# Kernel tuning notes

Hardware: AMD Instinct MI355X
Metric: run time of the kernel (lower is better)

The kernel has to match this reference:

```python
import jax, jax.numpy as jnp
import numpy as np

K = 5          # number of spline bins
B = 5.0        # tail bound
HIDDEN = 8
MIN_W = 1e-3; MIN_H = 1e-3; MIN_D = 1e-3  # RQS defaults (Durkan et al.)


def setup_inputs() -> dict:
    n, d = 32768, 64
    L = d - 1
    P = 3 * K - 1
    ks = jax.random.split(jax.random.key(0), 8)
    x = jax.random.normal(ks[0], (n, d), jnp.float32) * 2.0
    init_param = jax.random.uniform(ks[1], (P,), jnp.float32, -0.5, 0.5)
    # ragged first layers: layer l (predicts dim l+1) sees x[:, :l+1]; zero-pad to width L
    mask = (jnp.arange(L)[None, :] <= jnp.arange(L)[:, None]).astype(jnp.float32)
    W1 = jax.random.normal(ks[2], (L, L, HIDDEN), jnp.float32) * 0.2 * mask[:, :, None]
    b1 = jax.random.normal(ks[3], (L, HIDDEN), jnp.float32) * 0.1
    W2 = jax.random.normal(ks[4], (L, HIDDEN, HIDDEN), jnp.float32) * 0.2
    b2 = jax.random.normal(ks[5], (L, HIDDEN), jnp.float32) * 0.1
    W3 = jax.random.normal(ks[6], (L, HIDDEN, P), jnp.float32) * 0.2
    b3 = jax.random.normal(ks[7], (L, P), jnp.float32) * 0.1
    return {"x": x, "init_param": init_param, "W1": W1, "b1": b1,
            "W2": W2, "b2": b2, "W3": W3, "b3": b3}


def _rqs(xf, Wu, Hu, Du):
    # xf: (M,), Wu/Hu: (M,K), Du: (M,K-1) -- vectorized unconstrained RQS, forward
    inside = (xf >= -B) & (xf <= B)
    const = float(np.log(np.exp(1.0 - MIN_D) - 1.0))
    Dpad = jnp.pad(Du, ((0, 0), (1, 1)), constant_values=const)

    widths = MIN_W + (1.0 - MIN_W * K) * jax.nn.softmax(Wu, axis=-1)
    cumw = jnp.pad(jnp.cumsum(widths, -1), ((0, 0), (1, 0)))
    cumw = 2.0 * B * cumw - B
    cumw = cumw.at[:, 0].set(-B).at[:, -1].set(B)
    widths = cumw[:, 1:] - cumw[:, :-1]

    heights = MIN_H + (1.0 - MIN_H * K) * jax.nn.softmax(Hu, axis=-1)
    cumh = jnp.pad(jnp.cumsum(heights, -1), ((0, 0), (1, 0)))
    cumh = 2.0 * B * cumh - B
    cumh = cumh.at[:, 0].set(-B).at[:, -1].set(B)
    heights = cumh[:, 1:] - cumh[:, :-1]

    derivs = MIN_D + jax.nn.softplus(Dpad)  # (M, K+1)

    xc = jnp.clip(xf, -B, B)
    idx = jnp.clip(jnp.sum(xc[:, None] >= cumw, axis=-1) - 1, 0, K - 1)
    take = lambda a: jnp.take_along_axis(a, idx[:, None], axis=-1)[:, 0]

    icw, ibw = take(cumw), take(widths)
    ich, ih = take(cumh), take(heights)
    idl = take(heights / widths)
    idv = take(derivs)
    idvp1 = take(derivs[:, 1:])

    theta = (xc - icw) / ibw
    tmt = theta * (1.0 - theta)
    num = ih * (idl * theta * theta + idv * tmt)
    den = idl + (idv + idvp1 - 2.0 * idl) * tmt
    out = ich + num / den
    dnum = idl * idl * (idvp1 * theta * theta + 2.0 * idl * tmt + idv * (1.0 - theta) ** 2)
    ld = jnp.log(dnum) - 2.0 * jnp.log(den)
    return jnp.where(inside, out, xf), jnp.where(inside, ld, 0.0)


def reference(x, init_param, W1, b1, W2, b2, W3, b3):
    n, d = x.shape
    L = d - 1
    P = 3 * K - 1
    # mask re-applied so padded W1 entries are exactly inert (ragged Linear(i, hidden))
    mask = (jnp.arange(L)[None, :] <= jnp.arange(L)[:, None]).astype(x.dtype)
    h = jnp.tanh(jnp.einsum('nj,ljh->lnh', x[:, :L], W1 * mask[:, :, None]) + b1[:, None, :])
    h = jnp.tanh(jnp.einsum('lnh,lhg->lng', h, W2) + b2[:, None, :])
    out = jnp.einsum('lng,lgp->lnp', h, W3) + b3[:, None, :]      # (L, n, P)
    p0 = jnp.broadcast_to(init_param, (1, n, P))                  # dim 0 uses init_param
    params = jnp.concatenate([p0, out], axis=0).reshape(d * n, P)  # dim-major, matches Ws layout
    Wu, Hu, Du = params[:, :K], params[:, K:2 * K], params[:, 2 * K:]
    xf = x.T.reshape(-1)  # x.transpose(0,1).flatten()
    zs, lds = _rqs(xf, Wu, Hu, Du)
    # NOTE: faithfully replicates the original's reshape of the dim-major flat
    # vector directly to (n, d) (as in the torch source).
    return zs.reshape(n, d), lds.reshape(n, d).sum(axis=1)
```

## Files before the change

kernel.cpp:

```cpp
#include <hip/hip_runtime.h>
#include <hip/hip_bf16.h>
#include <math.h>

#define KK 5
#define Bc 5.0f
#define NN 32768
#define DD 64
#define LL 63
#define PP 14
#define MIN_Wc 0.001f
#define MIN_Hc 0.001f
#define MIN_Dc 0.001f

typedef float f4 __attribute__((ext_vector_type(4)));
typedef float f32x4 __attribute__((ext_vector_type(4)));
typedef float f2 __attribute__((ext_vector_type(2)));
typedef short short8 __attribute__((ext_vector_type(8)));

__device__ __forceinline__ float rcp_fast(float v)  { return __builtin_amdgcn_rcpf(v); }
__device__ __forceinline__ float exp_fast(float v)  { return __expf(v); }
__device__ __forceinline__ float log_fast(float v)  { return __logf(v); }
__device__ __forceinline__ float tanh_fast(float v) {
    float e = exp_fast(2.0f * v);
    return 1.0f - 2.0f * rcp_fast(e + 1.0f);
}
__device__ __forceinline__ float softplus_fast(float v) {
    return (v > 15.0f) ? v : log_fast(1.0f + exp_fast(v));
}
__device__ __forceinline__ ushort to_bf16u(float v) {
    __hip_bfloat16 b = __float2bfloat16(v);
    return *(ushort*)&b;
}
__device__ __forceinline__ f2 splat2(float v) { f2 r; r.x = v; r.y = v; return r; }
__device__ __forceinline__ f4 splat4(float v) { f4 r; r.x = v; r.y = v; r.z = v; r.w = v; return r; }

__global__ __launch_bounds__(256) void pack_b1(const float* __restrict__ W1,
                                               ushort* __restrict__ Bp) {
    int id = blockIdx.x * 256 + threadIdx.x;
    int n = id >> 6, k = id & 63;
    float v = 0.f;
    if (n < 504 && k < 63) {
        int l = n >> 3, h = n & 7;
        v = W1[(l * 63 + k) * 8 + h];
    }
    Bp[id] = to_bf16u(v);
}

__device__ __forceinline__ short8 pack_a(f4 v0, f4 v1) {
    short8 a;
    a[0] = (short)to_bf16u(v0.x); a[1] = (short)to_bf16u(v0.y);
    a[2] = (short)to_bf16u(v0.z); a[3] = (short)to_bf16u(v0.w);
    a[4] = (short)to_bf16u(v1.x); a[5] = (short)to_bf16u(v1.y);
    a[6] = (short)to_bf16u(v1.z); a[7] = (short)to_bf16u(v1.w);
    return a;
}

#define WSL 216

__device__ __forceinline__ void do_dim(
    int dd, const float* wp, float xf, uint4 hv, int s0, int lane, int bx,
    const float* __restrict__ init_param, float* __restrict__ out)
{
    float p0,p1,p2,p3,p4,p5,p6,p7,p8,p9,p10,p11,p12,p13;
    if (dd == 0) {
        p0 = init_param[0];  p1 = init_param[1];  p2 = init_param[2];
        p3 = init_param[3];  p4 = init_param[4];  p5 = init_param[5];
        p6 = init_param[6];  p7 = init_param[7];  p8 = init_param[8];
        p9 = init_param[9];  p10 = init_param[10]; p11 = init_param[11];
        p12 = init_param[12]; p13 = init_param[13];
    } else {
        float h1f[8];
        h1f[0] = __uint_as_float(hv.x << 16);
        h1f[1] = __uint_as_float(hv.x & 0xFFFF0000u);
        h1f[2] = __uint_as_float(hv.y << 16);
        h1f[3] = __uint_as_float(hv.y & 0xFFFF0000u);
        h1f[4] = __uint_as_float(hv.z << 16);
        h1f[5] = __uint_as_float(hv.z & 0xFFFF0000u);
        h1f[6] = __uint_as_float(hv.w << 16);
        h1f[7] = __uint_as_float(hv.w & 0xFFFF0000u);

        f4 h2a = *(const f4*)(wp + 64);
        f4 h2b = *(const f4*)(wp + 68);
        #pragma unroll
        for (int h = 0; h < 8; ++h) {
            f4 wa = *(const f4*)(wp + h * 8);
            f4 wb = *(const f4*)(wp + h * 8 + 4);
            f4 av = splat4(h1f[h]);
            h2a += av * wa;
            h2b += av * wb;
        }
        float h2f[8];
        h2f[0] = tanh_fast(h2a.x); h2f[1] = tanh_fast(h2a.y);
        h2f[2] = tanh_fast(h2a.z); h2f[3] = tanh_fast(h2a.w);
        h2f[4] = tanh_fast(h2b.x); h2f[5] = tanh_fast(h2b.y);
        h2f[6] = tanh_fast(h2b.z); h2f[7] = tanh_fast(h2b.w);

        f4 ppa = *(const f4*)(wp + 200);
        f4 ppb = *(const f4*)(wp + 204);
        f4 ppc = *(const f4*)(wp + 208);
        f4 ppd = *(const f4*)(wp + 212);
        #pragma unroll
        for (int g = 0; g < 8; ++g) {
            const float* wr = wp + 72 + g * 16;
            f4 w0 = *(const f4*)(wr);
            f4 w1 = *(const f4*)(wr + 4);
            f4 w2v = *(const f4*)(wr + 8);
            f4 w3v = *(const f4*)(wr + 12);
            f4 av = splat4(h2f[g]);
            ppa += av * w0;
            ppb += av * w1;
            ppc += av * w2v;
            ppd += av * w3v;
        }
        p0 = ppa.x; p1 = ppa.y; p2 = ppa.z; p3 = ppa.w;
        p4 = ppb.x; p5 = ppb.y; p6 = ppb.z; p7 = ppb.w;
        p8 = ppc.x; p9 = ppc.y; p10 = ppc.z; p11 = ppc.w;
        p12 = ppd.x; p13 = ppd.y;
    }

    f2 e0, e1, e2, e3, e4;
    e0.x = exp_fast(p0); e0.y = exp_fast(p5);
    e1.x = exp_fast(p1); e1.y = exp_fast(p6);
    e2.x = exp_fast(p2); e2.y = exp_fast(p7);
    e3.x = exp_fast(p3); e3.y = exp_fast(p8);
    e4.x = exp_fast(p4); e4.y = exp_fast(p9);
    f2 es = e0 + e1 + e2 + e3 + e4;
    f2 nrm; nrm.x = 0.995f * rcp_fast(es.x); nrm.y = 0.995f * rcp_fast(es.y);

    const f2 minv = {MIN_Wc, MIN_Hc};
    f2 cb0 = splat2(-Bc), acc2 = splat2(0.f);
    acc2 += minv + nrm * e0;  f2 cb1 = splat2(2.f * Bc) * acc2 - splat2(Bc);
    acc2 += minv + nrm * e1;  f2 cb2 = splat2(2.f * Bc) * acc2 - splat2(Bc);
    acc2 += minv + nrm * e2;  f2 cb3 = splat2(2.f * Bc) * acc2 - splat2(Bc);
    acc2 += minv + nrm * e3;  f2 cb4 = splat2(2.f * Bc) * acc2 - splat2(Bc);
    f2 cb5 = splat2(Bc);

    const float xc = fminf(fmaxf(xf, -Bc), Bc);

    float icw = cb0.x, ich = cb0.y;
    float ibw = cb1.x - cb0.x, ih = cb1.y - cb0.y;
    float rv = p10, rvp = p10;
    bool v_one = true, vp_one = false;
    {
        bool c = xc >= cb1.x; f2 dif = cb2 - cb1;
        icw = c ? cb1.x : icw; ich = c ? cb1.y : ich;
        ibw = c ? dif.x : ibw; ih  = c ? dif.y : ih;
        v_one = c ? false : v_one; rv = c ? p10 : rv; rvp = c ? p11 : rvp;
    }
    {
        bool c = xc >= cb2.x; f2 dif = cb3 - cb2;
        icw = c ? cb2.x : icw; ich = c ? cb2.y : ich;
        ibw = c ? dif.x : ibw; ih  = c ? dif.y : ih;
        rv = c ? p11 : rv; rvp = c ? p12 : rvp;
    }
    {
        bool c = xc >= cb3.x; f2 dif = cb4 - cb3;
        icw = c ? cb3.x : icw; ich = c ? cb3.y : ich;
        ibw = c ? dif.x : ibw; ih  = c ? dif.y : ih;
        rv = c ? p12 : rv; rvp = c ? p13 : rvp;
    }
    {
        bool c = xc >= cb4.x; f2 dif = cb5 - cb4;
        icw = c ? cb4.x : icw; ich = c ? cb4.y : ich;
        ibw = c ? dif.x : ibw; ih  = c ? dif.y : ih;
        rv = c ? p13 : rv; vp_one = c;
    }
    const float idv   = v_one  ? 1.0f : MIN_Dc + softplus_fast(rv);
    const float idvp1 = vp_one ? 1.0f : MIN_Dc + softplus_fast(rvp);

    const float ibw_r = rcp_fast(ibw);
    const float idl = ih * ibw_r;
    const float theta = (xc - icw) * ibw_r;
    const float omt = 1.0f - theta;
    const float tmt = theta * omt;
    const float num = ih * (idl * theta * theta + idv * tmt);
    const float den = idl + (idv + idvp1 - 2.0f * idl) * tmt;
    const float dr = rcp_fast(den);
    const float outv = ich + num * dr;
    const float dnum = idl * idl * (idvp1 * theta * theta + 2.0f * idl * tmt + idv * omt * omt);
    const float ld = log_fast(dnum * dr * dr);

    const bool inside = (xf >= -Bc) && (xf <= Bc);
    const float z = inside ? outv : xf;
    float ldv = inside ? ld : 0.0f;

    out[dd * NN + s0 + lane] = z;

    #pragma unroll
    for (int off = 32; off > 0; off >>= 1) ldv += __shfl_down(ldv, off);
    if (lane == 0) out[NN * DD + dd * (NN / 64) + bx] = ldv;
}

#define H1S 136
__global__ __launch_bounds__(256, 5) void fused_kernel(
    const float* __restrict__ x, const float* __restrict__ init_param,
    const ushort* __restrict__ Bp, const float* __restrict__ b1,
    const float* __restrict__ W2, const float* __restrict__ b2,
    const float* __restrict__ W3, const float* __restrict__ b3,
    float* __restrict__ out)
{
    __shared__ ushort h1c[64 * H1S];
    __shared__ float  wl[16 * WSL];
    const int tid = threadIdx.x;
    const int s0 = blockIdx.x * 64;
    const int y  = blockIdx.y;
    const int bx = blockIdx.x;
    const int lane = tid & 63;
    const int wave = __builtin_amdgcn_readfirstlane(tid >> 6);
    const int ln = lane & 15, qg = lane >> 4;
    const int m0 = wave * 16;
    const int l0 = y * 16;

    const float* xrow = x + (size_t)(s0 + lane) * 64;
    const int db = y * 16 + 1 + wave * 4;
    float xv0 = xrow[db];
    float xv1 = xrow[db + 1];
    float xv2 = xrow[db + 2];
    float xv3 = xrow[(y == 3 && wave == 3) ? 0 : db + 3];

    short8 a0, a1;
    {
        const float* xr = x + (size_t)(s0 + m0 + ln) * 64 + qg * 8;
        a0 = pack_a(*(const f4*)xr, *(const f4*)(xr + 4));
        a1 = (y >= 2) ? pack_a(*(const f4*)(xr + 32), *(const f4*)(xr + 36)) : a0;
    }

    {
        int s = tid >> 4, o = (tid & 15) * 4;
        if (l0 + s < LL)
            *(f4*)&wl[s * WSL + o] = *(const f4*)&W2[(l0 + s) * 64 + o];
    }
    if (tid < 128) {
        int s = tid >> 3, o = tid & 7;
        if (l0 + s < LL) wl[s * WSL + 64 + o] = b2[(l0 + s) * 8 + o];
    }
    #pragma unroll
    for (int q0 = 0; q0 < 896; q0 += 256) {
        int q = q0 + tid;
        if (q < 896) {
            int s = q / 56, r = q % 56, g = r / 7, o = r % 7;
            *(f2*)&wl[s * WSL + 72 + g * 16 + o * 2] =
                *(const f2*)&W3[(l0 + s) * 112 + g * 14 + o * 2];
        }
    }
    if (tid < 128) {
        int s = tid >> 3, g = tid & 7;
        *(f2*)&wl[s * WSL + 72 + g * 16 + 14] = splat2(0.f);
    }
    if (tid < 224) {
        int s = tid / 14, o = tid % 14;
        wl[s * WSL + 200 + o] = b3[(l0 + s < LL ? l0 + s : 0) * PP + o];
    }
    if (tid < 32) {
        int s = tid >> 1, o = 214 + (tid & 1);
        wl[s * WSL + o] = 0.f;
    }

    #pragma unroll
    for (int nt = 0; nt < 8; ++nt) {
        int ncol = y * 128 + nt * 16 + ln;
        const short8* bp8 = (const short8*)(Bp + ncol * 64 + qg * 8);
        f32x4 acc = {0.f, 0.f, 0.f, 0.f};
        acc = __builtin_amdgcn_mfma_f32_16x16x32_bf16(a0, bp8[0], acc, 0, 0, 0);
        if (y >= 2)
            acc = __builtin_amdgcn_mfma_f32_16x16x32_bf16(a1, bp8[4], acc, 0, 0, 0);
        float bias = (ncol < 504) ? b1[ncol] : 0.f;
        #pragma unroll
        for (int r = 0; r < 4; ++r) {
            float v = tanh_fast(acc[r] + bias);
            h1c[(m0 + qg * 4 + r) * H1S + nt * 16 + ln] = to_bf16u(v);
        }
    }
    __syncthreads();

    const uint4* hp = (const uint4*)&h1c[lane * H1S + wave * 32];
    uint4 hv0 = hp[0], hv1 = hp[1], hv2 = hp[2], hv3 = hp[3];

    const int sl = wave * 4;
    do_dim(db,     wl + (sl)     * WSL, xv0, hv0, s0, lane, bx, init_param, out);
    do_dim(db + 1, wl + (sl + 1) * WSL, xv1, hv1, s0, lane, bx, init_param, out);
    do_dim(db + 2, wl + (sl + 2) * WSL, xv2, hv2, s0, lane, bx, init_param, out);
    do_dim((y == 3 && wave == 3) ? 0 : db + 3,
                   wl + (sl + 3) * WSL, xv3, hv3, s0, lane, bx, init_param, out);
}

extern "C" void kernel_launch(void* const* d_in, const int* in_sizes, int n_in,
                              void* d_out, int out_size, void* d_ws, size_t ws_size,
                              hipStream_t stream) {
    const float* x          = (const float*)d_in[0];
    const float* init_param = (const float*)d_in[1];
    const float* W1         = (const float*)d_in[2];
    const float* b1         = (const float*)d_in[3];
    const float* W2         = (const float*)d_in[4];
    const float* b2         = (const float*)d_in[5];
    const float* W3         = (const float*)d_in[6];
    const float* b3         = (const float*)d_in[7];
    float* out = (float*)d_out;

    ushort* Bp = (ushort*)d_ws;

    pack_b1<<<128, 256, 0, stream>>>(W1, Bp);
    fused_kernel<<<dim3(512, 4), 256, 0, stream>>>(x, init_param, Bp, b1,
                                                   W2, b2, W3, b3, out);
}
```

Measured before the change: 111.1 us.

## Interleave two spline dims per call and fold tanh doubling into weights

Each thread now handles two dimensions at once in a paired routine, interleaving their MLP and spline arithmetic to expose more independent instructions and allow 4-wide packed ops on the cumulative bin computations. The factor of two inside tanh is pre-multiplied into W2, b2 and b1 when they are staged, which removes a multiply per tanh. The dim-0 branch now runs the MLP unconditionally and then overwrites the result with init_param, trading a little wasted work for less divergence. Register pressure rises because two dims' state is live at once.

```diff
diff --git a/kernel.cpp b/kernel.cpp
--- a/kernel.cpp
+++ b/kernel.cpp
@@ -20,8 +20,8 @@
 __device__ __forceinline__ float rcp_fast(float v)  { return __builtin_amdgcn_rcpf(v); }
 __device__ __forceinline__ float exp_fast(float v)  { return __expf(v); }
 __device__ __forceinline__ float log_fast(float v)  { return __logf(v); }
-__device__ __forceinline__ float tanh_fast(float v) {
-    float e = exp_fast(2.0f * v);
+__device__ __forceinline__ float tanh_pre(float t2) {
+    float e = exp_fast(t2);
     return 1.0f - 2.0f * rcp_fast(e + 1.0f);
 }
 __device__ __forceinline__ float softplus_fast(float v) {
@@ -57,138 +57,181 @@
 
 #define WSL 216
 
-__device__ __forceinline__ void do_dim(
-    int dd, const float* wp, float xf, uint4 hv, int s0, int lane, int bx,
-    const float* __restrict__ init_param, float* __restrict__ out)
+__device__ __forceinline__ void do_pair(
+    int ddA, int ddB, const float* wpA, const float* wpB,
+    float xfA, float xfB, uint4 hvA, uint4 hvB,
+    int s0, int lane, int bx,
+    const float* __restrict__ ip, float* __restrict__ out)
 {
-    float p0,p1,p2,p3,p4,p5,p6,p7,p8,p9,p10,p11,p12,p13;
-    if (dd == 0) {
-        p0 = init_param[0];  p1 = init_param[1];  p2 = init_param[2];
-        p3 = init_param[3];  p4 = init_param[4];  p5 = init_param[5];
-        p6 = init_param[6];  p7 = init_param[7];  p8 = init_param[8];
-        p9 = init_param[9];  p10 = init_param[10]; p11 = init_param[11];
-        p12 = init_param[12]; p13 = init_param[13];
-    } else {
-        float h1f[8];
-        h1f[0] = __uint_as_float(hv.x << 16);
-        h1f[1] = __uint_as_float(hv.x & 0xFFFF0000u);
-        h1f[2] = __uint_as_float(hv.y << 16);
-        h1f[3] = __uint_as_float(hv.y & 0xFFFF0000u);
-        h1f[4] = __uint_as_float(hv.z << 16);
-        h1f[5] = __uint_as_float(hv.z & 0xFFFF0000u);
-        h1f[6] = __uint_as_float(hv.w << 16);
-        h1f[7] = __uint_as_float(hv.w & 0xFFFF0000u);
-
-        f4 h2a = *(const f4*)(wp + 64);
-        f4 h2b = *(const f4*)(wp + 68);
+    float hA[8], hB[8];
+    hA[0] = __uint_as_float(hvA.x << 16);         hB[0] = __uint_as_float(hvB.x << 16);
+    hA[1] = __uint_as_float(hvA.x & 0xFFFF0000u); hB[1] = __uint_as_float(hvB.x & 0xFFFF0000u);
+    hA[2] = __uint_as_float(hvA.y << 16);         hB[2] = __uint_as_float(hvB.y << 16);
+    hA[3] = __uint_as_float(hvA.y & 0xFFFF0000u); hB[3] = __uint_as_float(hvB.y & 0xFFFF0000u);
+    hA[4] = __uint_as_float(hvA.z << 16);         hB[4] = __uint_as_float(hvB.z << 16);
+    hA[5] = __uint_as_float(hvA.z & 0xFFFF0000u); hB[5] = __uint_as_float(hvB.z & 0xFFFF0000u);
+    hA[6] = __uint_as_float(hvA.w << 16);         hB[6] = __uint_as_float(hvB.w << 16);
+    hA[7] = __uint_as_float(hvA.w & 0xFFFF0000u); hB[7] = __uint_as_float(hvB.w & 0xFFFF0000u);
+
+    f4 h2aA = *(const f4*)(wpA + 64), h2bA = *(const f4*)(wpA + 68);
+    f4 h2aB = *(const f4*)(wpB + 64), h2bB = *(const f4*)(wpB + 68);
+    #pragma unroll
+    for (int h = 0; h < 8; ++h) {
+        f4 avA = splat4(hA[h]);
+        f4 avB = splat4(hB[h]);
+        h2aA += avA * (*(const f4*)(wpA + h * 8));
+        h2aB += avB * (*(const f4*)(wpB + h * 8));
+        h2bA += avA * (*(const f4*)(wpA + h * 8 + 4));
+        h2bB += avB * (*(const f4*)(wpB + h * 8 + 4));
+    }
+    float g2A[8], g2B[8];
+    g2A[0] = tanh_pre(h2aA.x); g2B[0] = tanh_pre(h2aB.x);
+    g2A[1] = tanh_pre(h2aA.y); g2B[1] = tanh_pre(h2aB.y);
+    g2A[2] = tanh_pre(h2aA.z); g2B[2] = tanh_pre(h2aB.z);
+    g2A[3] = tanh_pre(h2aA.w); g2B[3] = tanh_pre(h2aB.w);
+    g2A[4] = tanh_pre(h2bA.x); g2B[4] = tanh_pre(h2bB.x);
+    g2A[5] = tanh_pre(h2bA.y); g2B[5] = tanh_pre(h2bB.y);
+    g2A[6] = tanh_pre(h2bA.z); g2B[6] = tanh_pre(h2bB.z);
+    g2A[7] = tanh_pre(h2bA.w); g2B[7] = tanh_pre(h2bB.w);
+
+    f4 paA = *(const f4*)(wpA + 200), pbA = *(const f4*)(wpA + 204);
+    f4 pcA = *(const f4*)(wpA + 208), pdA = *(const f4*)(wpA + 212);
+    f4 paB = *(const f4*)(wpB + 200), pbB = *(const f4*)(wpB + 204);
+    f4 pcB = *(const f4*)(wpB + 208), pdB = *(const f4*)(wpB + 212);
+    #pragma unroll
+    for (int g = 0; g < 8; ++g) {
+        const float* wrA = wpA + 72 + g * 16;
+        const float* wrB = wpB + 72 + g * 16;
+        f4 avA = splat4(g2A[g]);
+        f4 avB = splat4(g2B[g]);
+        paA += avA * (*(const f4*)(wrA));
+        paB += avB * (*(const f4*)(wrB));
+        pbA += avA * (*(const f4*)(wrA + 4));
+        pbB += avB * (*(const f4*)(wrB + 4));
+        pcA += avA * (*(const f4*)(wrA + 8));
+        pcB += avB * (*(const f4*)(wrB + 8));
+        pdA += avA * (*(const f4*)(wrA + 12));
+        pdB += avB * (*(const f4*)(wrB + 12));
+    }
+    float pA[PP], pB[PP];
+    pA[0]=paA.x; pA[1]=paA.y; pA[2]=paA.z; pA[3]=paA.w;
+    pA[4]=pbA.x; pA[5]=pbA.y; pA[6]=pbA.z; pA[7]=pbA.w;
+    pA[8]=pcA.x; pA[9]=pcA.y; pA[10]=pcA.z; pA[11]=pcA.w;
+    pA[12]=pdA.x; pA[13]=pdA.y;
+    pB[0]=paB.x; pB[1]=paB.y; pB[2]=paB.z; pB[3]=paB.w;
+    pB[4]=pbB.x; pB[5]=pbB.y; pB[6]=pbB.z; pB[7]=pbB.w;
+    pB[8]=pcB.x; pB[9]=pcB.y; pB[10]=pcB.z; pB[11]=pcB.w;
+    pB[12]=pdB.x; pB[13]=pdB.y;
+
+    if (ddA == 0) {
         #pragma unroll
-        for (int h = 0; h < 8; ++h) {
-            f4 wa = *(const f4*)(wp + h * 8);
-            f4 wb = *(const f4*)(wp + h * 8 + 4);
-            f4 av = splat4(h1f[h]);
-            h2a += av * wa;
-            h2b += av * wb;
-        }
-        float h2f[8];
-        h2f[0] = tanh_fast(h2a.x); h2f[1] = tanh_fast(h2a.y);
-        h2f[2] = tanh_fast(h2a.z); h2f[3] = tanh_fast(h2a.w);
-        h2f[4] = tanh_fast(h2b.x); h2f[5] = tanh_fast(h2b.y);
-        h2f[6] = tanh_fast(h2b.z); h2f[7] = tanh_fast(h2b.w);
-
-        f4 ppa = *(const f4*)(wp + 200);
-        f4 ppb = *(const f4*)(wp + 204);
-        f4 ppc = *(const f4*)(wp + 208);
-        f4 ppd = *(const f4*)(wp + 212);
+        for (int i = 0; i < PP; ++i) pA[i] = ip[i];
+    }
+    if (ddB == 0) {
         #pragma unroll
-        for (int g = 0; g < 8; ++g) {
-            const float* wr = wp + 72 + g * 16;
-            f4 w0 = *(const f4*)(wr);
-            f4 w1 = *(const f4*)(wr + 4);
-            f4 w2v = *(const f4*)(wr + 8);
-            f4 w3v = *(const f4*)(wr + 12);
-            f4 av = splat4(h2f[g]);
-            ppa += av * w0;
-            ppb += av * w1;
-            ppc += av * w2v;
-            ppd += av * w3v;
-        }
-        p0 = ppa.x; p1 = ppa.y; p2 = ppa.z; p3 = ppa.w;
-        p4 = ppb.x; p5 = ppb.y; p6 = ppb.z; p7 = ppb.w;
-        p8 = ppc.x; p9 = ppc.y; p10 = ppc.z; p11 = ppc.w;
-        p12 = ppd.x; p13 = ppd.y;
-    }
-
-    f2 e0, e1, e2, e3, e4;
-    e0.x = exp_fast(p0); e0.y = exp_fast(p5);
-    e1.x = exp_fast(p1); e1.y = exp_fast(p6);
-    e2.x = exp_fast(p2); e2.y = exp_fast(p7);
-    e3.x = exp_fast(p3); e3.y = exp_fast(p8);
-    e4.x = exp_fast(p4); e4.y = exp_fast(p9);
-    f2 es = e0 + e1 + e2 + e3 + e4;
-    f2 nrm; nrm.x = 0.995f * rcp_fast(es.x); nrm.y = 0.995f * rcp_fast(es.y);
-
-    const f2 minv = {MIN_Wc, MIN_Hc};
-    f2 cb0 = splat2(-Bc), acc2 = splat2(0.f);
-    acc2 += minv + nrm * e0;  f2 cb1 = splat2(2.f * Bc) * acc2 - splat2(Bc);
-    acc2 += minv + nrm * e1;  f2 cb2 = splat2(2.f * Bc) * acc2 - splat2(Bc);
-    acc2 += minv + nrm * e2;  f2 cb3 = splat2(2.f * Bc) * acc2 - splat2(Bc);
-    acc2 += minv + nrm * e3;  f2 cb4 = splat2(2.f * Bc) * acc2 - splat2(Bc);
-    f2 cb5 = splat2(Bc);
-
-    const float xc = fminf(fmaxf(xf, -Bc), Bc);
-
-    float icw = cb0.x, ich = cb0.y;
-    float ibw = cb1.x - cb0.x, ih = cb1.y - cb0.y;
-    float rv = p10, rvp = p10;
-    bool v_one = true, vp_one = false;
-    {
-        bool c = xc >= cb1.x; f2 dif = cb2 - cb1;
-        icw = c ? cb1.x : icw; ich = c ? cb1.y : ich;
-        ibw = c ? dif.x : ibw; ih  = c ? dif.y : ih;
-        v_one = c ? false : v_one; rv = c ? p10 : rv; rvp = c ? p11 : rvp;
-    }
-    {
-        bool c = xc >= cb2.x; f2 dif = cb3 - cb2;
-        icw = c ? cb2.x : icw; ich = c ? cb2.y : ich;
-        ibw = c ? dif.x : ibw; ih  = c ? dif.y : ih;
-        rv = c ? p11 : rv; rvp = c ? p12 : rvp;
-    }
-    {
-        bool c = xc >= cb3.x; f2 dif = cb4 - cb3;
-        icw = c ? cb3.x : icw; ich = c ? cb3.y : ich;
-        ibw = c ? dif.x : ibw; ih  = c ? dif.y : ih;
-        rv = c ? p12 : rv; rvp = c ? p13 : rvp;
-    }
-    {
-        bool c = xc >= cb4.x; f2 dif = cb5 - cb4;
-        icw = c ? cb4.x : icw; ich = c ? cb4.y : ich;
-        ibw = c ? dif.x : ibw; ih  = c ? dif.y : ih;
-        rv = c ? p13 : rv; vp_one = c;
-    }
-    const float idv   = v_one  ? 1.0f : MIN_Dc + softplus_fast(rv);
-    const float idvp1 = vp_one ? 1.0f : MIN_Dc + softplus_fast(rvp);
-
-    const float ibw_r = rcp_fast(ibw);
-    const float idl = ih * ibw_r;
-    const float theta = (xc - icw) * ibw_r;
-    const float omt = 1.0f - theta;
-    const float tmt = theta * omt;
-    const float num = ih * (idl * theta * theta + idv * tmt);
-    const float den = idl + (idv + idvp1 - 2.0f * idl) * tmt;
-    const float dr = rcp_fast(den);
-    const float outv = ich + num * dr;
-    const float dnum = idl * idl * (idvp1 * theta * theta + 2.0f * idl * tmt + idv * omt * omt);
-    const float ld = log_fast(dnum * dr * dr);
-
-    const bool inside = (xf >= -Bc) && (xf <= Bc);
-    const float z = inside ? outv : xf;
-    float ldv = inside ? ld : 0.0f;
-
-    out[dd * NN + s0 + lane] = z;
-
-    #pragma unroll
-    for (int off = 32; off > 0; off >>= 1) ldv += __shfl_down(ldv, off);
-    if (lane == 0) out[NN * DD + dd * (NN / 64) + bx] = ldv;
+        for (int i = 0; i < PP; ++i) pB[i] = ip[i];
+    }
+
+    f4 e0, e1, e2, e3, e4;
+    e0.x = exp_fast(pA[0]); e0.y = exp_fast(pA[5]); e0.z = exp_fast(pB[0]); e0.w = exp_fast(pB[5]);
+    e1.x = exp_fast(pA[1]); e1.y = exp_fast(pA[6]); e1.z = exp_fast(pB[1]); e1.w = exp_fast(pB[6]);
+    e2.x = exp_fast(pA[2]); e2.y = exp_fast(pA[7]); e2.z = exp_fast(pB[2]); e2.w = exp_fast(pB[7]);
+    e3.x = exp_fast(pA[3]); e3.y = exp_fast(pA[8]); e3.z = exp_fast(pB[3]); e3.w = exp_fast(pB[8]);
+    e4.x = exp_fast(pA[4]); e4.y = exp_fast(pA[9]); e4.z = exp_fast(pB[4]); e4.w = exp_fast(pB[9]);
+    f4 es = (e0 + e1) + (e2 + e3) + e4;
+    f4 nrm;
+    nrm.x = 0.995f * rcp_fast(es.x); nrm.y = 0.995f * rcp_fast(es.y);
+    nrm.z = 0.995f * rcp_fast(es.z); nrm.w = 0.995f * rcp_fast(es.w);
+
+    const f4 minv = {MIN_Wc, MIN_Hc, MIN_Wc, MIN_Hc};
+    f4 acc4 = splat4(0.f);
+    acc4 += minv + nrm * e0;  f4 cb1 = splat4(2.f * Bc) * acc4 - splat4(Bc);
+    acc4 += minv + nrm * e1;  f4 cb2 = splat4(2.f * Bc) * acc4 - splat4(Bc);
+    acc4 += minv + nrm * e2;  f4 cb3 = splat4(2.f * Bc) * acc4 - splat4(Bc);
+    acc4 += minv + nrm * e3;  f4 cb4 = splat4(2.f * Bc) * acc4 - splat4(Bc);
+
+    const float xcA = fminf(fmaxf(xfA, -Bc), Bc);
+    const float xcB = fminf(fmaxf(xfB, -Bc), Bc);
+
+    float icwA = -Bc, ichA = -Bc, ibwA = cb1.x + Bc, ihA = cb1.y + Bc;
+    float icwB = -Bc, ichB = -Bc, ibwB = cb1.z + Bc, ihB = cb1.w + Bc;
+    float rvA = pA[10], rvpA = pA[10], rvB = pB[10], rvpB = pB[10];
+    bool voneA = true, vponeA = false, voneB = true, vponeB = false;
+    {
+        bool cA = xcA >= cb1.x;                bool cB = xcB >= cb1.z;
+        icwA = cA ? cb1.x : icwA;              icwB = cB ? cb1.z : icwB;
+        ichA = cA ? cb1.y : ichA;              ichB = cB ? cb1.w : ichB;
+        ibwA = cA ? cb2.x - cb1.x : ibwA;      ibwB = cB ? cb2.z - cb1.z : ibwB;
+        ihA  = cA ? cb2.y - cb1.y : ihA;       ihB  = cB ? cb2.w - cb1.w : ihB;
+        voneA = cA ? false : voneA;            voneB = cB ? false : voneB;
+        rvA  = cA ? pA[10] : rvA;              rvB  = cB ? pB[10] : rvB;
+        rvpA = cA ? pA[11] : rvpA;             rvpB = cB ? pB[11] : rvpB;
+    }
+    {
+        bool cA = xcA >= cb2.x;                bool cB = xcB >= cb2.z;
+        icwA = cA ? cb2.x : icwA;              icwB = cB ? cb2.z : icwB;
+        ichA = cA ? cb2.y : ichA;              ichB = cB ? cb2.w : ichB;
+        ibwA = cA ? cb3.x - cb2.x : ibwA;      ibwB = cB ? cb3.z - cb2.z : ibwB;
+        ihA  = cA ? cb3.y - cb2.y : ihA;       ihB  = cB ? cb3.w - cb2.w : ihB;
+        rvA  = cA ? pA[11] : rvA;              rvB  = cB ? pB[11] : rvB;
+        rvpA = cA ? pA[12] : rvpA;             rvpB = cB ? pB[12] : rvpB;
+    }
+    {
+        bool cA = xcA >= cb3.x;                bool cB = xcB >= cb3.z;
+        icwA = cA ? cb3.x : icwA;              icwB = cB ? cb3.z : icwB;
+        ichA = cA ? cb3.y : ichA;              ichB = cB ? cb3.w : ichB;
+        ibwA = cA ? cb4.x - cb3.x : ibwA;      ibwB = cB ? cb4.z - cb3.z : ibwB;
+        ihA  = cA ? cb4.y - cb3.y : ihA;       ihB  = cB ? cb4.w - cb3.w : ihB;
+        rvA  = cA ? pA[12] : rvA;              rvB  = cB ? pB[12] : rvB;
+        rvpA = cA ? pA[13] : rvpA;             rvpB = cB ? pB[13] : rvpB;
+    }
+    {
+        bool cA = xcA >= cb4.x;                bool cB = xcB >= cb4.z;
+        icwA = cA ? cb4.x : icwA;              icwB = cB ? cb4.z : icwB;
+        ichA = cA ? cb4.y : ichA;              ichB = cB ? cb4.w : ichB;
+        ibwA = cA ? Bc - cb4.x : ibwA;         ibwB = cB ? Bc - cb4.z : ibwB;
+        ihA  = cA ? Bc - cb4.y : ihA;          ihB  = cB ? Bc - cb4.w : ihB;
+        rvA  = cA ? pA[13] : rvA;              rvB  = cB ? pB[13] : rvB;
+        vponeA = cA;                           vponeB = cB;
+    }
+    const float idvA   = voneA  ? 1.0f : MIN_Dc + softplus_fast(rvA);
+    const float idvB   = voneB  ? 1.0f : MIN_Dc + softplus_fast(rvB);
+    const float idvp1A = vponeA ? 1.0f : MIN_Dc + softplus_fast(rvpA);
+    const float idvp1B = vponeB ? 1.0f : MIN_Dc + softplus_fast(rvpB);
+
+    const float ibrA = rcp_fast(ibwA);         const float ibrB = rcp_fast(ibwB);
+    const float idlA = ihA * ibrA;             const float idlB = ihB * ibrB;
+    const float thA = (xcA - icwA) * ibrA;     const float thB = (xcB - icwB) * ibrB;
+    const float omA = 1.0f - thA;              const float omB = 1.0f - thB;
+    const float tmA = thA * omA;               const float tmB = thB * omB;
+    const float numA = ihA * (idlA * thA * thA + idvA * tmA);
+    const float numB = ihB * (idlB * thB * thB + idvB * tmB);
+    const float denA = idlA + (idvA + idvp1A - 2.0f * idlA) * tmA;
+    const float denB = idlB + (idvB + idvp1B - 2.0f * idlB) * tmB;
+    const float drA = rcp_fast(denA);          const float drB = rcp_fast(denB);
+    const float outA = ichA + numA * drA;      const float outB = ichB + numB * drB;
+    const float dnA = idlA * idlA * (idvp1A * thA * thA + 2.0f * idlA * tmA + idvA * omA * omA);
+    const float dnB = idlB * idlB * (idvp1B * thB * thB + 2.0f * idlB * tmB + idvB * omB * omB);
+    const float ldA = log_fast(dnA * drA * drA);
+    const float ldB = log_fast(dnB * drB * drB);
+
+    const bool inA = (xfA >= -Bc) && (xfA <= Bc);
+    const bool inB = (xfB >= -Bc) && (xfB <= Bc);
+    const float zA = inA ? outA : xfA;         const float zB = inB ? outB : xfB;
+    float lvA = inA ? ldA : 0.0f;              float lvB = inB ? ldB : 0.0f;
+
+    out[ddA * NN + s0 + lane] = zA;
+    out[ddB * NN + s0 + lane] = zB;
+
+    #pragma unroll
+    for (int off = 32; off > 0; off >>= 1) {
+        lvA += __shfl_down(lvA, off);
+        lvB += __shfl_down(lvB, off);
+    }
+    if (lane == 0) {
+        out[NN * DD + ddA * (NN / 64) + bx] = lvA;
+        out[NN * DD + ddB * (NN / 64) + bx] = lvB;
+    }
 }
 
 #define H1S 136
@@ -228,19 +271,20 @@
     {
         int s = tid >> 4, o = (tid & 15) * 4;
         if (l0 + s < LL)
-            *(f4*)&wl[s * WSL + o] = *(const f4*)&W2[(l0 + s) * 64 + o];
+            *(f4*)&wl[s * WSL + o] = splat4(2.f) * (*(const f4*)&W2[(l0 + s) * 64 + o]);
     }
     if (tid < 128) {
         int s = tid >> 3, o = tid & 7;
-        if (l0 + s < LL) wl[s * WSL + 64 + o] = b2[(l0 + s) * 8 + o];
+        if (l0 + s < LL) wl[s * WSL + 64 + o] = 2.f * b2[(l0 + s) * 8 + o];
     }
     #pragma unroll
     for (int q0 = 0; q0 < 896; q0 += 256) {
         int q = q0 + tid;
         if (q < 896) {
             int s = q / 56, r = q % 56, g = r / 7, o = r % 7;
-            *(f2*)&wl[s * WSL + 72 + g * 16 + o * 2] =
-                *(const f2*)&W3[(l0 + s) * 112 + g * 14 + o * 2];
+            if (l0 + s < LL)
+                *(f2*)&wl[s * WSL + 72 + g * 16 + o * 2] =
+                    *(const f2*)&W3[(l0 + s) * 112 + g * 14 + o * 2];
         }
     }
     if (tid < 128) {
@@ -264,10 +308,10 @@
         acc = __builtin_amdgcn_mfma_f32_16x16x32_bf16(a0, bp8[0], acc, 0, 0, 0);
         if (y >= 2)
             acc = __builtin_amdgcn_mfma_f32_16x16x32_bf16(a1, bp8[4], acc, 0, 0, 0);
-        float bias = (ncol < 504) ? b1[ncol] : 0.f;
+        float bias2 = (ncol < 504) ? 2.f * b1[ncol] : 0.f;
         #pragma unroll
         for (int r = 0; r < 4; ++r) {
-            float v = tanh_fast(acc[r] + bias);
+            float v = tanh_pre(fmaf(2.0f, acc[r], bias2));
             h1c[(m0 + qg * 4 + r) * H1S + nt * 16 + ln] = to_bf16u(v);
         }
     }
@@ -277,11 +321,12 @@
     uint4 hv0 = hp[0], hv1 = hp[1], hv2 = hp[2], hv3 = hp[3];
 
     const int sl = wave * 4;
-    do_dim(db,     wl + (sl)     * WSL, xv0, hv0, s0, lane, bx, init_param, out);
-    do_dim(db + 1, wl + (sl + 1) * WSL, xv1, hv1, s0, lane, bx, init_param, out);
-    do_dim(db + 2, wl + (sl + 2) * WSL, xv2, hv2, s0, lane, bx, init_param, out);
-    do_dim((y == 3 && wave == 3) ? 0 : db + 3,
-                   wl + (sl + 3) * WSL, xv3, hv3, s0, lane, bx, init_param, out);
+    do_pair(db, db + 1,
+            wl + sl * WSL, wl + (sl + 1) * WSL,
+            xv0, xv1, hv0, hv1, s0, lane, bx, init_param, out);
+    do_pair(db + 2, (y == 3 && wave == 3) ? 0 : db + 3,
+            wl + (sl + 2) * WSL, wl + (sl + 3) * WSL,
+            xv2, xv3, hv2, hv3, s0, lane, bx, init_param, out);
 }
 
 extern "C" void kernel_launch(void* const* d_in, const int* in_sizes, int n_in,
```

Measured after the change: 426.9 us. +284.2%, slower.
